# Optimization experiments

Measured on AMD Instinct MI355X. Metric: run time of the kernel, lower is better.

The kernel has to match this reference:

```python
import jax, jax.numpy as jnp
import numpy as np

D_MODEL = 1024
N_HEADS = 16
HEAD_DIM = D_MODEL // N_HEADS
WINDOW = 256


def setup_inputs() -> dict:
    key = jax.random.key(0)
    ks = jax.random.split(key, 5)
    s = 1.0 / np.sqrt(D_MODEL)
    x = jax.random.normal(ks[0], (1, 4096, D_MODEL), dtype=jnp.float32)
    W_qkv = jax.random.uniform(ks[1], (D_MODEL, 3 * D_MODEL), jnp.float32, -s, s)
    b_qkv = jax.random.uniform(ks[2], (3 * D_MODEL,), jnp.float32, -s, s)
    W_proj = jax.random.uniform(ks[3], (D_MODEL, D_MODEL), jnp.float32, -s, s)
    b_proj = jax.random.uniform(ks[4], (D_MODEL,), jnp.float32, -s, s)
    return {"x": x, "W_qkv": W_qkv, "b_qkv": b_qkv, "W_proj": W_proj, "b_proj": b_proj}


def reference(x, W_qkv, b_qkv, W_proj, b_proj):
    b, t, c = x.shape
    qkv = x @ W_qkv + b_qkv  # [b,t,3c]
    q, k, v = jnp.split(qkv, 3, axis=-1)
    # [b,h,t,d]
    q = q.reshape(b, t, N_HEADS, HEAD_DIM).transpose(0, 2, 1, 3)
    k = k.reshape(b, t, N_HEADS, HEAD_DIM).transpose(0, 2, 1, 3)
    v = v.reshape(b, t, N_HEADS, HEAD_DIM).transpose(0, 2, 1, 3)
    att = jnp.einsum('bhqd,bhkd->bhqk', q, k) / np.sqrt(HEAD_DIM)
    idx = jnp.arange(t)
    diff = idx[:, None] - idx[None, :]  # query - key
    allowed = (diff >= 0) & (diff < WINDOW)  # causal & local window
    att = jnp.where(allowed[None, None], att, -jnp.inf)
    att = jax.nn.softmax(att, axis=-1)
    y = jnp.einsum('bhqk,bhkd->bhqd', att, v)
    y = y.transpose(0, 2, 1, 3).reshape(b, t, c)
    return y @ W_proj + b_proj
```

## Files before the change

### kernel.cpp

```cpp
#include <hip/hip_runtime.h>
#include <stdint.h>

#define TSEQ 4096
#define DMODEL 1024
#define N3 3072
#define NHEADS 16
#define HDIM 64
#define WINDOW 256

typedef __attribute__((ext_vector_type(8))) short short8;
typedef __attribute__((ext_vector_type(4))) float f32x4;

__device__ __forceinline__ unsigned short f2bf(float f) {
  unsigned u = __builtin_bit_cast(unsigned, f);
  return (unsigned short)((u + 0x7fffu + ((u >> 16) & 1u)) >> 16);
}

__device__ __forceinline__ unsigned cvtpk(float lo, float hi) {
  unsigned r;
  asm("v_cvt_pk_bf16_f32 %0, %1, %2" : "=v"(r) : "v"(lo), "v"(hi));
  return r;
}

__device__ __forceinline__ f32x4 mfma16(short8 a, short8 b, f32x4 c) {
  return __builtin_amdgcn_mfma_f32_16x16x32_bf16(a, b, c, 0, 0, 0);
}

__device__ __forceinline__ void g2lds16(const void* g, void* l) {
  __builtin_amdgcn_global_load_lds(
      (const __attribute__((address_space(1))) void*)(uintptr_t)g,
      (__attribute__((address_space(3))) void*)(uintptr_t)l,
      16, 0, 0);
}


__global__ __launch_bounds__(256) void prep(const float* __restrict__ x,
                                            const float* __restrict__ Wqkv,
                                            const float* __restrict__ Wproj,
                                            unsigned short* __restrict__ xb,
                                            unsigned short* __restrict__ oQkvT,
                                            unsigned short* __restrict__ oProjT) {
  __shared__ float tile[32][33];
  int b = blockIdx.x;
  int tid = threadIdx.x;
  if (b < 4096) {
    int i = (b * 256 + tid) * 4;
    float4 v = *(const float4*)(x + i);
    unsigned lo = cvtpk(v.x, v.y), hi = cvtpk(v.z, v.w);
    unsigned long long packed = (unsigned long long)lo | ((unsigned long long)hi << 32);
    *(unsigned long long*)(xb + i) = packed;
    return;
  }
  b -= 4096;
  int bx = b & 127, by = b >> 7;
  const float* in;
  unsigned short* out;
  int C;
  if (bx < 96) {
    in = Wqkv; out = oQkvT; C = N3;
  } else {
    bx -= 96; in = Wproj; out = oProjT; C = DMODEL;
  }
  const int R = DMODEL;
  int c0 = bx * 32;
  int r0 = by * 32;
  int tx = tid & 31, ty = tid >> 5;
#pragma unroll
  for (int i = 0; i < 32; i += 8)
    tile[ty + i][tx] = in[(size_t)(r0 + ty + i) * C + c0 + tx];
  __syncthreads();
#pragma unroll
  for (int i = 0; i < 32; i += 8)
    out[(size_t)(c0 + ty + i) * R + r0 + tx] = f2bf(tile[tx][ty + i]);
}


__global__ __launch_bounds__(512, 2)
void gemm_qkv_256(const unsigned short* __restrict__ A,
                  const unsigned short* __restrict__ BT,
                  const float* __restrict__ bias,
                  unsigned short* __restrict__ oQ,
                  unsigned short* __restrict__ oK,
                  unsigned short* __restrict__ oVT) {
  __shared__ unsigned short Asm[2][256 * 64];
  __shared__ unsigned short Bsm[2][256 * 64];
  int m0 = blockIdx.x * 256;
  int n0 = blockIdx.y * 256;
  int tid = threadIdx.x;
  int w = tid >> 6, lane = tid & 63;
  int l15 = lane & 15, l4 = lane >> 4;
  int wr = w >> 2, wc = w & 3;

  f32x4 acc[8][4];
#pragma unroll
  for (int i = 0; i < 8; i++)
#pragma unroll
    for (int j = 0; j < 4; j++) acc[i][j] = (f32x4){0.f, 0.f, 0.f, 0.f};

  int r8 = lane >> 3;
  int sslot = ((lane & 7) ^ r8) * 16;
  const char* aBase = (const char*)A + (size_t)(m0 + r8) * 2048 + sslot;
  const char* bBase = (const char*)BT + (size_t)(n0 + r8) * 2048 + sslot;

  auto stage = [&](int T, int b) {
    int koff = T * 128;
#pragma unroll
    for (int u = 0; u < 2; u++)
#pragma unroll
      for (int j = 0; j < 2; j++) {
        int R0 = u * 128 + w * 16 + j * 8;
        g2lds16(aBase + (size_t)R0 * 2048 + koff, &Asm[b][R0 * 64]);
        g2lds16(bBase + (size_t)R0 * 2048 + koff, &Bsm[b][R0 * 64]);
      }
  };

  int xw = (l15 & 7) << 4;

  auto computeIter = [&](int b) {
    const char* Ab = (const char*)Asm[b];
    const char* Bb = (const char*)Bsm[b];
    short8 bfr[4][2];
#pragma unroll
    for (int ni = 0; ni < 4; ni++) {
      int rb = (wc * 64 + ni * 16 + l15) * 128;
#pragma unroll
      for (int ks = 0; ks < 2; ks++)
        bfr[ni][ks] = *(const short8*)(Bb + rb + ((ks * 64 + l4 * 16) ^ xw));
    }
#pragma unroll
    for (int p = 0; p < 4; p++) {
      short8 af[2][2];
#pragma unroll
      for (int i = 0; i < 2; i++) {
        int ra = (wr * 128 + (p * 2 + i) * 16 + l15) * 128;
#pragma unroll
        for (int ks = 0; ks < 2; ks++)
          af[i][ks] = *(const short8*)(Ab + ra + ((ks * 64 + l4 * 16) ^ xw));
      }
      __builtin_amdgcn_s_setprio(1);
#pragma unroll
      for (int i = 0; i < 2; i++)
#pragma unroll
        for (int ni = 0; ni < 4; ni++) {
          acc[p * 2 + i][ni] = mfma16(af[i][0], bfr[ni][0], acc[p * 2 + i][ni]);
          acc[p * 2 + i][ni] = mfma16(af[i][1], bfr[ni][1], acc[p * 2 + i][ni]);
        }
      __builtin_amdgcn_s_setprio(0);
      __builtin_amdgcn_sched_barrier(0);
    }
  };

  const int NT = 16;
  stage(0, 0);
#pragma unroll 1
  for (int T = 0; T < NT; T++) {
    asm volatile("s_waitcnt vmcnt(0)" ::: "memory");
    __builtin_amdgcn_s_barrier();
    if (T + 1 < NT) stage(T + 1, (T + 1) & 1);
    computeIter(T & 1);
  }

#pragma unroll
  for (int ni = 0; ni < 4; ni++) {
    int nn = n0 + wc * 64 + ni * 16 + l15;
    float bv = bias[nn];
    int c = nn & 1023;
    int hh = c >> 6, dd = c & 63;
#pragma unroll
    for (int mi = 0; mi < 8; mi++) {
      int mm = m0 + wr * 128 + mi * 16 + l4 * 4;
      float v0 = acc[mi][ni][0] + bv;
      float v1 = acc[mi][ni][1] + bv;
      float v2 = acc[mi][ni][2] + bv;
      float v3 = acc[mi][ni][3] + bv;
      if (nn < 1024) {
        oQ[((size_t)hh * TSEQ + mm + 0) * 64 + dd] = f2bf(v0 * 0.125f);
        oQ[((size_t)hh * TSEQ + mm + 1) * 64 + dd] = f2bf(v1 * 0.125f);
        oQ[((size_t)hh * TSEQ + mm + 2) * 64 + dd] = f2bf(v2 * 0.125f);
        oQ[((size_t)hh * TSEQ + mm + 3) * 64 + dd] = f2bf(v3 * 0.125f);
      } else if (nn < 2048) {
        oK[((size_t)hh * TSEQ + mm + 0) * 64 + dd] = f2bf(v0);
        oK[((size_t)hh * TSEQ + mm + 1) * 64 + dd] = f2bf(v1);
        oK[((size_t)hh * TSEQ + mm + 2) * 64 + dd] = f2bf(v2);
        oK[((size_t)hh * TSEQ + mm + 3) * 64 + dd] = f2bf(v3);
      } else {
        unsigned lo = cvtpk(v0, v1), hi = cvtpk(v2, v3);
        unsigned long long pv = (unsigned long long)lo | ((unsigned long long)hi << 32);
        *(unsigned long long*)(oVT + ((size_t)hh * 64 + dd) * TSEQ + mm) = pv;
      }
    }
  }
}


template <int EPI, int MI, int NI>
__global__ __launch_bounds__(256)
void gemm_bf16(const unsigned short* __restrict__ A,
               const unsigned short* __restrict__ BT,
               const float* __restrict__ bias,
               unsigned short* __restrict__ oQ,
               unsigned short* __restrict__ oK,
               unsigned short* __restrict__ oVT,
               float* __restrict__ oF) {
  constexpr int BM = MI * 32, BN = NI * 32;
  constexpr int LPS = MI / 2 + NI / 2;
  __shared__ unsigned short Asm[2][BM * 32];
  __shared__ unsigned short Bsm[2][BN * 32];
  const int K = 1024;
  int m0 = blockIdx.x * BM;
  int n0 = blockIdx.y * BN;
  int tid = threadIdx.x;
  int w = tid >> 6, lane = tid & 63;
  int l15 = lane & 15, l4 = lane >> 4;
  int wm = (w >> 1) * (MI * 16), wn = (w & 1) * (NI * 16);

  f32x4 acc[MI][NI];
#pragma unroll
  for (int i = 0; i < MI; i++)
#pragma unroll
    for (int j = 0; j < NI; j++) acc[i][j] = (f32x4){0.f, 0.f, 0.f, 0.f};

  int lr = lane >> 2;
  int slot = ((lane & 3) * 16) ^ (((lr >> 1) & 3) << 4);
  const char* aG = (const char*)(A + (size_t)(m0 + w * (MI * 8) + lr) * K) + slot;
  const char* bG = (const char*)(BT + (size_t)(n0 + w * (NI * 8) + lr) * K) + slot;

  auto stage = [&](int s, int b) {
    int koff = s * 64;
#pragma unroll
    for (int c = 0; c < MI / 2; c++)
      g2lds16(aG + (size_t)c * 16 * 2048 + koff, &Asm[b][(w * (MI / 2) + c) * 512]);
#pragma unroll
    for (int j = 0; j < NI / 2; j++)
      g2lds16(bG + (size_t)j * 16 * 2048 + koff, &Bsm[b][(w * (NI / 2) + j) * 512]);
  };

  int sX = ((l15 >> 1) & 3) << 4;

  auto compute = [&](int b) {
    short8 af[MI], bfr[NI];
#pragma unroll
    for (int mi = 0; mi < MI; mi++) {
      int rA = wm + mi * 16 + l15;
      af[mi] = *(const short8*)((const char*)Asm[b] + rA * 64 + ((l4 * 16) ^ sX));
    }
#pragma unroll
    for (int ni = 0; ni < NI; ni++) {
      int rB = wn + ni * 16 + l15;
      bfr[ni] = *(const short8*)((const char*)Bsm[b] + rB * 64 + ((l4 * 16) ^ sX));
    }
#pragma unroll
    for (int mi = 0; mi < MI; mi++)
#pragma unroll
      for (int ni = 0; ni < NI; ni++)
        acc[mi][ni] = mfma16(af[mi], bfr[ni], acc[mi][ni]);
  };

  const int NS = K / 32;
  stage(0, 0);
#pragma unroll 1
  for (int s = 0; s < NS; s++) {
    if (s + 1 < NS) {
      stage(s + 1, (s + 1) & 1);
      if constexpr (LPS == 4) asm volatile("s_waitcnt vmcnt(4)" ::: "memory");
      else asm volatile("s_waitcnt vmcnt(2)" ::: "memory");
    } else {
      asm volatile("s_waitcnt vmcnt(0)" ::: "memory");
    }
    __builtin_amdgcn_s_barrier();
    __builtin_amdgcn_sched_barrier(0);
    compute(s & 1);
    __builtin_amdgcn_sched_barrier(0);
    __builtin_amdgcn_s_barrier();
  }

#pragma unroll
  for (int ni = 0; ni < NI; ni++) {
    int nn = n0 + wn + ni * 16 + l15;
    float bv = bias[nn];
#pragma unroll
    for (int mi = 0; mi < MI; mi++) {
      int mm = m0 + wm + mi * 16 + l4 * 4;
#pragma unroll
      for (int r = 0; r < 4; r++)
        oF[(size_t)(mm + r) * 1024 + nn] = acc[mi][ni][r] + bv;
    }
  }
}


__global__ __launch_bounds__(512)
void attn_swa(const unsigned short* __restrict__ Qa,
              const unsigned short* __restrict__ Ka,
              const unsigned short* __restrict__ Vt,
              unsigned short* __restrict__ Y) {
  __shared__ __align__(16) char KV[2][16384];
  __shared__ __align__(16) unsigned char Pl[8][2048];
  int flat = blockIdx.x;
  int swz = (flat & 7) * 64 + (flat >> 3);
  int h = swz >> 5, qb2 = swz & 31;
  int w = threadIdx.x >> 6, lane = threadIdx.x & 63;
  int l15 = lane & 15, l4 = lane >> 4;
  int g = w >> 2, wv = w & 3;
  int qb = qb2 * 2 + g;
  int qrow0 = qb * 64 + wv * 16;
  int q = qrow0 + l15;

  const unsigned short* qp = Qa + ((size_t)h * TSEQ + q) * 64 + l4 * 8;
  short8 qf0 = *(const short8*)qp;
  short8 qf1 = *(const short8*)(qp + 32);

  const char* kgb = (const char*)(Ka + (size_t)h * TSEQ * 64);
  const char* vgb = (const char*)(Vt + (size_t)h * 64 * TSEQ);

  int sub8 = lane >> 3, slot = (lane & 7) * 16;
  int r8 = w * 8 + sub8;
  auto stage = [&](int kt, int b) {
    int kbase = kt * 64;
    g2lds16(kgb + (size_t)(kbase + r8) * 128 + (slot ^ (sub8 << 4)), &KV[b][w * 1024]);
    g2lds16(vgb + (size_t)r8 * 8192 + (size_t)kbase * 2 + (slot ^ (sub8 << 4)),
            &KV[b][8192 + w * 1024]);
  };

  float m = -1e30f, lsum = 0.f;
  f32x4 o[4];
#pragma unroll
  for (int ni = 0; ni < 4; ni++) o[ni] = (f32x4){0.f, 0.f, 0.f, 0.f};

  unsigned char* pw = Pl[w];
  int xw = (l15 & 7) << 4;

  auto compute = [&](int kt, int b, int MODE) {
    int kbase = kt * 64;
    const char* kb = KV[b];
    const char* vb = KV[b] + 8192;
    f32x4 s[4];
    __builtin_amdgcn_s_setprio(1);
#pragma unroll
    for (int ni = 0; ni < 4; ni++) {
      int rb = (ni * 16 + l15) * 128;
      short8 k0 = *(const short8*)(kb + rb + ((l4 * 16) ^ xw));
      short8 k1 = *(const short8*)(kb + rb + ((64 + l4 * 16) ^ xw));
      f32x4 z = (f32x4){0.f, 0.f, 0.f, 0.f};
      z = mfma16(k0, qf0, z);
      s[ni] = mfma16(k1, qf1, z);
    }
    __builtin_amdgcn_s_setprio(0);
    if (MODE != 0) {
#pragma unroll
      for (int ni = 0; ni < 4; ni++)
#pragma unroll
        for (int r = 0; r < 4; r++) {
          int key = kbase + ni * 16 + l4 * 4 + r;
          bool ok = (MODE == 2) ? (key <= q) : (q - key < WINDOW);
          s[ni][r] = ok ? s[ni][r] : -1e30f;
        }
    }
    float pm0 = fmaxf(fmaxf(s[0][0], s[0][1]), fmaxf(s[0][2], s[0][3]));
    float pm1 = fmaxf(fmaxf(s[1][0], s[1][1]), fmaxf(s[1][2], s[1][3]));
    float pm2 = fmaxf(fmaxf(s[2][0], s[2][1]), fmaxf(s[2][2], s[2][3]));
    float pm3 = fmaxf(fmaxf(s[3][0], s[3][1]), fmaxf(s[3][2], s[3][3]));
    float pm = fmaxf(fmaxf(pm0, pm1), fmaxf(pm2, pm3));
    pm = fmaxf(pm, __shfl_xor(pm, 16, 64));
    pm = fmaxf(pm, __shfl_xor(pm, 32, 64));
    if (!__all(pm <= m)) {
      float mn = fmaxf(m, pm);
      float alpha = __expf(m - mn);
      m = mn;
      lsum *= alpha;
#pragma unroll
      for (int ni = 0; ni < 4; ni++)
#pragma unroll
        for (int r = 0; r < 4; r++) o[ni][r] *= alpha;
    }
    float rs = 0.f;
#pragma unroll
    for (int ni = 0; ni < 4; ni++)
#pragma unroll
      for (int r = 0; r < 4; r++) {
        float p = __expf(s[ni][r] - m);
        s[ni][r] = p;
        rs += p;
      }
    rs += __shfl_xor(rs, 16, 64);
    rs += __shfl_xor(rs, 32, 64);
    lsum += rs;
#pragma unroll
    for (int ni = 0; ni < 4; ni++) {
      unsigned lo = cvtpk(s[ni][0], s[ni][1]);
      unsigned hi = cvtpk(s[ni][2], s[ni][3]);
      unsigned long long pv = (unsigned long long)lo | ((unsigned long long)hi << 32);
      *(unsigned long long*)(pw + l15 * 128 + ((ni * 32 + l4 * 8) ^ xw)) = pv;
    }
    short8 pa0 = *(const short8*)(pw + l15 * 128 + ((l4 * 16) ^ xw));
    short8 pa1 = *(const short8*)(pw + l15 * 128 + ((64 + l4 * 16) ^ xw));
    __builtin_amdgcn_s_setprio(1);
#pragma unroll
    for (int ni = 0; ni < 4; ni++) {
      int rb = (ni * 16 + l15) * 128;
      short8 v0 = *(const short8*)(vb + rb + ((l4 * 16) ^ xw));
      short8 v1 = *(const short8*)(vb + rb + ((64 + l4 * 16) ^ xw));
      o[ni] = mfma16(v0, pa0, o[ni]);
      o[ni] = mfma16(v1, pa1, o[ni]);
    }
    __builtin_amdgcn_s_setprio(0);
  };

  int qbA = qb2 * 2, qbB = qbA + 1;
  int ktLo = qbA >= 4 ? qbA - 4 : 0;
  int NT = qbB - ktLo + 1;
  stage(ktLo, 0);
  for (int t = 0; t < NT; t++) {
    int kt = ktLo + t;
    if (t + 1 < NT) {
      stage(kt + 1, (t + 1) & 1);
      asm volatile("s_waitcnt vmcnt(2)" ::: "memory");
    } else {
      asm volatile("s_waitcnt vmcnt(0)" ::: "memory");
    }
    __builtin_amdgcn_s_barrier();
    __builtin_amdgcn_sched_barrier(0);
    bool active = (g == 0) ? (kt <= qbA) : (kt >= qbB - 4);
    if (active) {
      int MODE = (kt == qb) ? 2 : ((qb >= 4 && kt == qb - 4) ? 1 : 0);
      compute(kt, t & 1, MODE);
    }
    __builtin_amdgcn_sched_barrier(0);
    __builtin_amdgcn_s_barrier();
  }

  float inv = 1.f / lsum;
#pragma unroll
  for (int ni = 0; ni < 4; ni++) {
    unsigned lo = cvtpk(o[ni][0] * inv, o[ni][1] * inv);
    unsigned hi = cvtpk(o[ni][2] * inv, o[ni][3] * inv);
    unsigned long long yv = (unsigned long long)lo | ((unsigned long long)hi << 32);
    *(unsigned long long*)(Y + (size_t)q * DMODEL + h * 64 + ni * 16 + l4 * 4) = yv;
  }
}


extern "C" void kernel_launch(void* const* d_in, const int* in_sizes, int n_in,
                              void* d_out, int out_size, void* d_ws, size_t ws_size,
                              hipStream_t stream) {
  const float* x = (const float*)d_in[0];
  const float* Wqkv = (const float*)d_in[1];
  const float* bqkv = (const float*)d_in[2];
  const float* Wproj = (const float*)d_in[3];
  const float* bproj = (const float*)d_in[4];
  float* out = (float*)d_out;

  unsigned short* ws = (unsigned short*)d_ws;
  unsigned short* xb = ws;
  unsigned short* wqkvT = xb + (size_t)TSEQ * DMODEL;
  unsigned short* wprojT = wqkvT + (size_t)N3 * DMODEL;
  unsigned short* qarr = wprojT + (size_t)DMODEL * DMODEL;
  unsigned short* karr = qarr + (size_t)NHEADS * TSEQ * HDIM;
  unsigned short* vtarr = karr + (size_t)NHEADS * TSEQ * HDIM;
  unsigned short* yarr = vtarr + (size_t)NHEADS * TSEQ * HDIM;

  prep<<<8192, 256, 0, stream>>>(x, Wqkv, Wproj, xb, wqkvT, wprojT);
  gemm_qkv_256<<<dim3(TSEQ / 256, N3 / 256), 512, 0, stream>>>(
      xb, wqkvT, bqkv, qarr, karr, vtarr);
  attn_swa<<<512, 512, 0, stream>>>(qarr, karr, vtarr, yarr);
  gemm_bf16<1, 2, 2><<<dim3(TSEQ / 64, DMODEL / 64), 256, 0, stream>>>(
      yarr, wprojT, bproj, nullptr, nullptr, nullptr, out);
}
```

Before: 84.65 us.

## Restructure QKV GEMM into 8-phase pipeline with half-K LDS tiles and prefetch

The QKV projection GEMM now splits each 64-wide K tile into two 32-wide halves held in separate LDS buffers. Global-to-LDS loads are issued per quarter-phase, running up to two K tiles ahead, and waits use vmcnt(10) instead of draining to zero each iteration. The goal is to overlap memory traffic with MFMA work instead of stalling on a full vmcnt(0) wait. In exchange it adds more barriers per iteration, a new swizzle, and fragile hand-counted waitcnt values that must match the number of loads in flight.

```diff
diff --git a/kernel.cpp b/kernel.cpp
--- a/kernel.cpp
+++ b/kernel.cpp
@@ -76,14 +76,14 @@
 
 
 __global__ __launch_bounds__(512, 2)
-void gemm_qkv_256(const unsigned short* __restrict__ A,
+void gemm_qkv_8ph(const unsigned short* __restrict__ A,
                   const unsigned short* __restrict__ BT,
                   const float* __restrict__ bias,
                   unsigned short* __restrict__ oQ,
                   unsigned short* __restrict__ oK,
                   unsigned short* __restrict__ oVT) {
-  __shared__ unsigned short Asm[2][256 * 64];
-  __shared__ unsigned short Bsm[2][256 * 64];
+  __shared__ unsigned short Ah[2][2][256 * 32];
+  __shared__ unsigned short Bh[2][2][256 * 32];
   int m0 = blockIdx.x * 256;
   int n0 = blockIdx.y * 256;
   int tid = threadIdx.x;
@@ -97,67 +97,70 @@
 #pragma unroll
     for (int j = 0; j < 4; j++) acc[i][j] = (f32x4){0.f, 0.f, 0.f, 0.f};
 
-  int r8 = lane >> 3;
-  int sslot = ((lane & 7) ^ r8) * 16;
-  const char* aBase = (const char*)A + (size_t)(m0 + r8) * 2048 + sslot;
-  const char* bBase = (const char*)BT + (size_t)(n0 + r8) * 2048 + sslot;
-
-  auto stage = [&](int T, int b) {
-    int koff = T * 128;
-#pragma unroll
-    for (int u = 0; u < 2; u++)
-#pragma unroll
-      for (int j = 0; j < 2; j++) {
-        int R0 = u * 128 + w * 16 + j * 8;
-        g2lds16(aBase + (size_t)R0 * 2048 + koff, &Asm[b][R0 * 64]);
-        g2lds16(bBase + (size_t)R0 * 2048 + koff, &Bsm[b][R0 * 64]);
+  int lr = lane >> 2;
+  int slot = ((lane & 3) * 16) ^ (((lr >> 1) & 3) << 4);
+  const char* aB = (const char*)A + (size_t)(m0 + w * 16 + lr) * 2048 + slot;
+  const char* bB = (const char*)BT + (size_t)(n0 + w * 16 + lr) * 2048 + slot;
+  const size_t c128 = (size_t)128 * 2048;
+
+  auto stageA = [&](int Tt, int ks) {
+    int off = Tt * 128 + ks * 64;
+    g2lds16(aB + off, &Ah[Tt & 1][ks][(w * 16) * 32]);
+    g2lds16(aB + c128 + off, &Ah[Tt & 1][ks][(128 + w * 16) * 32]);
+  };
+  auto stageB = [&](int Tt, int ks) {
+    int off = Tt * 128 + ks * 64;
+    g2lds16(bB + off, &Bh[Tt & 1][ks][(w * 16) * 32]);
+    g2lds16(bB + c128 + off, &Bh[Tt & 1][ks][(128 + w * 16) * 32]);
+  };
+
+  int sX = ((l15 >> 1) & 3) << 4;
+
+  stageA(0, 0); stageB(0, 0); stageA(0, 1); stageB(0, 1);
+  stageA(1, 0); stageB(1, 0); stageA(1, 1);
+  asm volatile("s_waitcnt vmcnt(10)" ::: "memory");
+  __builtin_amdgcn_s_barrier();
+
+  const int NT = 16;
+  short8 af[8];
+#pragma unroll 1
+  for (int T = 0; T < NT; T++) {
+    int bu = T & 1;
+#pragma unroll
+    for (int q = 0; q < 4; q++) {
+      const int ks = q >> 1, np = q & 1;
+      short8 bfr[2];
+      if (np == 0) {
+        const char* Ab = (const char*)Ah[bu][ks];
+#pragma unroll
+        for (int mi = 0; mi < 8; mi++)
+          af[mi] = *(const short8*)(Ab + (wr * 128 + mi * 16 + l15) * 64 + ((l4 * 16) ^ sX));
       }
-  };
-
-  int xw = (l15 & 7) << 4;
-
-  auto computeIter = [&](int b) {
-    const char* Ab = (const char*)Asm[b];
-    const char* Bb = (const char*)Bsm[b];
-    short8 bfr[4][2];
-#pragma unroll
-    for (int ni = 0; ni < 4; ni++) {
-      int rb = (wc * 64 + ni * 16 + l15) * 128;
-#pragma unroll
-      for (int ks = 0; ks < 2; ks++)
-        bfr[ni][ks] = *(const short8*)(Bb + rb + ((ks * 64 + l4 * 16) ^ xw));
-    }
-#pragma unroll
-    for (int p = 0; p < 4; p++) {
-      short8 af[2][2];
-#pragma unroll
-      for (int i = 0; i < 2; i++) {
-        int ra = (wr * 128 + (p * 2 + i) * 16 + l15) * 128;
-#pragma unroll
-        for (int ks = 0; ks < 2; ks++)
-          af[i][ks] = *(const short8*)(Ab + ra + ((ks * 64 + l4 * 16) ^ xw));
+      {
+        const char* Bb = (const char*)Bh[bu][ks];
+#pragma unroll
+        for (int j = 0; j < 2; j++)
+          bfr[j] = *(const short8*)(Bb + (wc * 64 + (np * 2 + j) * 16 + l15) * 64 + ((l4 * 16) ^ sX));
       }
+      if (q == 0) { if (T + 1 < NT) stageB(T + 1, 1); }
+      else if (q == 1) { if (T + 2 < NT) stageA(T + 2, 0); }
+      else if (q == 2) { if (T + 2 < NT) stageB(T + 2, 0); }
+      else { if (T + 2 < NT) stageA(T + 2, 1); }
+      __builtin_amdgcn_s_barrier();
+      asm volatile("s_waitcnt lgkmcnt(0)" ::: "memory");
+      __builtin_amdgcn_sched_barrier(0);
       __builtin_amdgcn_s_setprio(1);
 #pragma unroll
-      for (int i = 0; i < 2; i++)
-#pragma unroll
-        for (int ni = 0; ni < 4; ni++) {
-          acc[p * 2 + i][ni] = mfma16(af[i][0], bfr[ni][0], acc[p * 2 + i][ni]);
-          acc[p * 2 + i][ni] = mfma16(af[i][1], bfr[ni][1], acc[p * 2 + i][ni]);
-        }
+      for (int mi = 0; mi < 8; mi++)
+#pragma unroll
+        for (int j = 0; j < 2; j++)
+          acc[mi][np * 2 + j] = mfma16(af[mi], bfr[j], acc[mi][np * 2 + j]);
       __builtin_amdgcn_s_setprio(0);
       __builtin_amdgcn_sched_barrier(0);
-    }
-  };
-
-  const int NT = 16;
-  stage(0, 0);
-#pragma unroll 1
-  for (int T = 0; T < NT; T++) {
-    asm volatile("s_waitcnt vmcnt(0)" ::: "memory");
-    __builtin_amdgcn_s_barrier();
-    if (T + 1 < NT) stage(T + 1, (T + 1) & 1);
-    computeIter(T & 1);
+      if (np == 1)
+        asm volatile("s_waitcnt vmcnt(10)" ::: "memory");
+      __builtin_amdgcn_s_barrier();
+    }
   }
 
 #pragma unroll
@@ -460,7 +463,7 @@
   unsigned short* yarr = vtarr + (size_t)NHEADS * TSEQ * HDIM;
 
   prep<<<8192, 256, 0, stream>>>(x, Wqkv, Wproj, xb, wqkvT, wprojT);
-  gemm_qkv_256<<<dim3(TSEQ / 256, N3 / 256), 512, 0, stream>>>(
+  gemm_qkv_8ph<<<dim3(TSEQ / 256, N3 / 256), 512, 0, stream>>>(
       xb, wqkvT, bqkv, qarr, karr, vtarr);
   attn_swa<<<512, 512, 0, stream>>>(qarr, karr, vtarr, yarr);
   gemm_bf16<1, 2, 2><<<dim3(TSEQ / 64, DMODEL / 64), 256, 0, stream>>>(
```

Measured after the change: 87.30 us. 1.03x slower.
